# Performance work log

Measured on AMD Instinct MI355X. Metric: run time of the kernel, lower is better.

Reference implementation:

```python
import jax, jax.numpy as jnp
import numpy as np

K = 128            # knowledge_n == stu_dim == prednet_input_len
EXER = 16384       # exer_n
N = K + EXER       # entity count
B = 4096           # batch of students
E = 400000         # edges per graph
T = B * 50         # packed history length (avg 50 interactions/student)


def setup_inputs() -> dict:
    key = jax.random.key(0)
    ks = jax.random.split(key, 24)
    f = lambda i, shape: jax.random.normal(ks[i], shape, dtype=jnp.float32) * 0.05
    inp = {
        # learned parameters
        'entity_emb': f(0, (N, K)),
        'gcn_W': f(1, (3, 4, K, K)),          # 3 graphs x 4 layers
        'gcn_b': jnp.zeros((3, 4, K), jnp.float32),
        'full_stu_W': f(2, (2 * K,)),          # Linear(2K -> 1) weight
        'full_stu_b': f(3, ()),
        'full_exer_W': f(4, (2 * K,)),
        'full_exer_b': f(5, ()),
        'disc_emb': f(6, (EXER, 1)),           # e_discrimination embedding
        'W1': f(7, (K, 512)), 'b1': jnp.zeros((512,), jnp.float32),
        'W2': f(8, (512, 216)), 'b2': jnp.zeros((216,), jnp.float32),
        'W3': f(9, (216, 1)), 'b3': jnp.zeros((1,), jnp.float32),
        # graph structure (local_map), edge lists over all N entities
        'sim_src': jax.random.randint(ks[10], (E,), 0, N),
        'sim_dst': jax.random.randint(ks[11], (E,), 0, N),
        'pre_src': jax.random.randint(ks[12], (E,), 0, N),
        'pre_dst': jax.random.randint(ks[13], (E,), 0, N),
        'ec_src': jax.random.randint(ks[14], (E,), 0, N),
        'ec_dst': jax.random.randint(ks[15], (E,), 0, N),
        # forward args
        'stu_id': jax.random.randint(ks[16], (B,), 0, 8192),
        'exer_id': jax.random.randint(ks[17], (B,), 0, EXER),
        'kn_emb': jax.random.uniform(ks[18], (B, K), dtype=jnp.float32),
        'history_ids': jax.random.randint(ks[19], (T,), 0, EXER),
        'history_segids': jnp.sort(jax.random.randint(ks[20], (T,), 0, B)),
    }
    return inp


def _edge_norm(src, dst, n):
    ones = jnp.ones(src.shape[0], jnp.float32)
    deg_o = jax.ops.segment_sum(ones, src, num_segments=n)
    deg_i = jax.ops.segment_sum(ones, dst, num_segments=n)
    return jax.lax.rsqrt(jnp.maximum(deg_o[src], 1.0) * jnp.maximum(deg_i[dst], 1.0))


def reference(entity_emb, gcn_W, gcn_b, full_stu_W, full_stu_b, full_exer_W,
              full_exer_b, disc_emb, W1, b1, W2, b2, W3, b3,
              sim_src, sim_dst, pre_src, pre_dst, ec_src, ec_dst,
              stu_id, exer_id, kn_emb, history_ids, history_segids):
    graphs = [(sim_src, sim_dst), (pre_src, pre_dst), (ec_src, ec_dst)]
    norms = [_edge_norm(s, d, N) for s, d in graphs]

    # 4-layer, 3-graph GCN diffusion over entity embeddings
    embs = [entity_emb]
    h = entity_emb
    for l in range(4):
        nh = jnp.zeros_like(h)
        for g, (s, d) in enumerate(graphs):
            agg = jax.ops.segment_sum(h[s] * norms[g][:, None], d, num_segments=N)
            nh = nh + agg @ gcn_W[g, l] + gcn_b[g, l]
        h = nh
        embs.append(h)
    stack = jnp.stack(embs)                       # [5, N, K]
    full = jnp.mean(stack, axis=0)
    disc_full = jnp.mean(stack[3:], axis=0)       # discarding_layers=2 -> layers 3,4

    concept = full[:K]                            # [K, K]
    exer_ent = full[K:]                           # [EXER, K]
    stu_exe = disc_full[K:]                       # [EXER, K]

    # ragged per-student history gather + mean (packed segment reduce)
    Bn = stu_id.shape[0]
    ssum = jax.ops.segment_sum(stu_exe[history_ids], history_segids, num_segments=Bn)
    cnt = jax.ops.segment_sum(jnp.ones(history_ids.shape[0], jnp.float32),
                              history_segids, num_segments=Bn)
    stu = ssum / jnp.maximum(cnt, 1.0)[:, None]   # [B, K]

    exer = exer_ent[exer_id]                      # [B, K]

    # broadcast bilinear: cat(repeat(x), kn_vector) @ W  ==  xWa + conceptWb + b
    prof = jax.nn.sigmoid((stu @ full_stu_W[:K])[:, None]
                          + (concept @ full_stu_W[K:])[None, :] + full_stu_b)
    diff = jax.nn.sigmoid((exer @ full_exer_W[:K])[:, None]
                          + (concept @ full_exer_W[K:])[None, :] + full_exer_b)
    e_disc = jax.nn.sigmoid(disc_emb[exer_id]) * 10.0   # [B, 1]

    x = e_disc * (prof - diff) * kn_emb           # [B, K]
    x = jax.nn.sigmoid(x @ W1 + b1)
    x = jax.nn.sigmoid(x @ W2 + b2)
    return jax.nn.sigmoid(x @ W3 + b3)            # [B, 1]
```

## Files before the change

### kernel.cpp

```cpp
#include <hip/hip_runtime.h>

constexpr int KDIM  = 128;
constexpr int NEXER = 16384;
constexpr int NNODE = KDIM + NEXER;
constexpr int NEDGE = 400000;
constexpr int NBATCH = 4096;
constexpr int NHIST = NBATCH * 50;

constexpr int NCHUNK = 32;
constexpr int CHSZ   = NEDGE / NCHUNK;
constexpr int RHALF  = NNODE / 2;

typedef __attribute__((ext_vector_type(8))) short bf16x8;
typedef __attribute__((ext_vector_type(4))) float f32x4;

__device__ __forceinline__ float sigmoidf(float x) {
    return 1.0f / (1.0f + __expf(-x));
}

__device__ __forceinline__ ushort f2bf(float f) {
    uint x = __float_as_uint(f);
    uint r = (x + 0x7FFFu + ((x >> 16) & 1u)) >> 16;
    return (ushort)r;
}

__device__ __forceinline__ void accum8(float* ax, uint4 p, float w) {
    ax[0] += w * __uint_as_float(p.x << 16);
    ax[1] += w * __uint_as_float(p.x & 0xFFFF0000u);
    ax[2] += w * __uint_as_float(p.y << 16);
    ax[3] += w * __uint_as_float(p.y & 0xFFFF0000u);
    ax[4] += w * __uint_as_float(p.z << 16);
    ax[5] += w * __uint_as_float(p.z & 0xFFFF0000u);
    ax[6] += w * __uint_as_float(p.w << 16);
    ax[7] += w * __uint_as_float(p.w & 0xFFFF0000u);
}

__global__ __launch_bounds__(256) void prep_emb_kernel(
    const float* __restrict__ entity, ushort* __restrict__ h_bf,
    float* __restrict__ full_acc)
{
    int idx = blockIdx.x * 256 + threadIdx.x;
    if (idx >= NNODE * KDIM / 2) return;
    float2 v = ((const float2*)entity)[idx];
    ((float2*)full_acc)[idx] = v;
    ((uint*)h_bf)[idx] = (uint)f2bf(v.x) | ((uint)f2bf(v.y) << 16);
}

__global__ __launch_bounds__(256) void prep_w_kernel(
    const float* __restrict__ W, ushort* __restrict__ Wt)
{
    __shared__ float tile[32][33];
    int gl = blockIdx.y;
    int tk = blockIdx.x >> 2, tn = blockIdx.x & 3;
    int k0 = tk * 32, n0 = tn * 32;
    int tx = threadIdx.x & 31, ty = threadIdx.x >> 5;
    const float* src = W + ((size_t)gl << 14);
    #pragma unroll
    for (int i = 0; i < 4; ++i) {
        int k = ty * 4 + i;
        tile[k][tx] = src[(k0 + k) * 128 + n0 + tx];
    }
    __syncthreads();
    ushort* dst = Wt + ((size_t)gl << 14);
    #pragma unroll
    for (int i = 0; i < 4; ++i) {
        int n = ty * 4 + i;
        dst[(n0 + n) * 128 + k0 + tx] = f2bf(tile[tx][n]);
    }
}

__global__ __launch_bounds__(256) void prep_head_kernel(
    const float* __restrict__ W1, const float* __restrict__ W2,
    ushort* __restrict__ W1t, ushort* __restrict__ W2t)
{
    int idx = blockIdx.x * 256 + threadIdx.x;
    if (idx < 512 * 128) {
        int n = idx >> 7, k = idx & 127;
        W1t[idx] = f2bf(W1[k * 512 + n]);
    }
    int idx2 = idx - 512 * 128;
    if (idx2 >= 0 && idx2 < 224 * 512) {
        int n = idx2 >> 9, k = idx2 & 511;
        W2t[idx2] = f2bf(n < 216 ? W2[k * 216 + n] : 0.f);
    }
}

__global__ __launch_bounds__(256) void count_part_kernel(
    const int* __restrict__ s0, const int* __restrict__ d0,
    const int* __restrict__ s1, const int* __restrict__ d1,
    const int* __restrict__ s2, const int* __restrict__ d2,
    int* __restrict__ partial,
    ushort* __restrict__ rank)
{
    __shared__ int hist[RHALF];
    int c = blockIdx.x, r = blockIdx.y, gs = blockIdx.z;
    const int* arr = (gs == 0) ? s0 : (gs == 1) ? d0 : (gs == 2) ? s1
                   : (gs == 3) ? d1 : (gs == 4) ? s2 : d2;
    for (int i = threadIdx.x; i < RHALF; i += 256) hist[i] = 0;
    __syncthreads();
    int base = r * RHALF;
    const int* p = arr + c * CHSZ;
    if (gs & 1) {
        ushort* rk = rank + (size_t)(gs >> 1) * NEDGE + c * CHSZ;
        for (int i = threadIdx.x; i < CHSZ; i += 256) {
            int v = p[i] - base;
            if ((unsigned)v < (unsigned)RHALF)
                rk[i] = (ushort)atomicAdd(&hist[v], 1);
        }
    } else {
        for (int i = threadIdx.x; i < CHSZ; i += 256) {
            int v = p[i] - base;
            if ((unsigned)v < (unsigned)RHALF) atomicAdd(&hist[v], 1);
        }
    }
    __syncthreads();
    int* outp = partial + ((size_t)gs * NCHUNK + c) * NNODE + base;
    for (int i = threadIdx.x; i < RHALF; i += 256) outp[i] = hist[i];
}

__global__ __launch_bounds__(256) void sum_kernel(
    const int* __restrict__ partial, int* __restrict__ cnt)
{
    int idx = blockIdx.x * 256 + threadIdx.x;
    if (idx >= 6 * NNODE) return;
    int gs = idx / NNODE, node = idx - gs * NNODE;
    const int* pp = partial + (size_t)gs * NCHUNK * NNODE + node;
    int s = 0;
    #pragma unroll
    for (int c = 0; c < NCHUNK; ++c) s += pp[c * NNODE];
    cnt[idx] = s;
}

__global__ __launch_bounds__(256) void scan_kernel(
    const int* __restrict__ cnt, int* __restrict__ rp)
{
    int g = blockIdx.x;
    const int* c = cnt + (g * 2 + 1) * NNODE;
    int* r = rp + g * (NNODE + 1);
    __shared__ int part[256];
    int t = threadIdx.x;
    constexpr int CH = (NNODE + 255) / 256;
    int lo = t * CH;
    int hi = lo + CH; if (hi > NNODE) hi = NNODE;
    int s = 0;
    for (int i = lo; i < hi; ++i) s += c[i];
    part[t] = s;
    __syncthreads();
    for (int off = 1; off < 256; off <<= 1) {
        int v = part[t];
        if (t >= off) v += part[t - off];
        __syncthreads();
        part[t] = v;
        __syncthreads();
    }
    int run = (t == 0) ? 0 : part[t - 1];
    for (int i = lo; i < hi; ++i) { r[i] = run; run += c[i]; }
    if (t == 255) r[NNODE] = part[255];
}

__global__ __launch_bounds__(256) void base_kernel(
    const int* __restrict__ partial, const int* __restrict__ rp,
    int* __restrict__ chunk_base)
{
    int idx = blockIdx.x * 256 + threadIdx.x;
    if (idx >= 3 * NNODE) return;
    int g = idx / NNODE, node = idx - g * NNODE;
    int running = rp[g * (NNODE + 1) + node];
    const int* pp = partial + (size_t)(g * 2 + 1) * NCHUNK * NNODE + node;
    int* ob = chunk_base + (size_t)g * NCHUNK * NNODE + node;
    #pragma unroll
    for (int c = 0; c < NCHUNK; ++c) { ob[c * NNODE] = running; running += pp[c * NNODE]; }
}

__global__ __launch_bounds__(256) void fill_scatter_kernel(
    const int* __restrict__ s0, const int* __restrict__ d0,
    const int* __restrict__ s1, const int* __restrict__ d1,
    const int* __restrict__ s2, const int* __restrict__ d2,
    const int* __restrict__ cnt, const int* __restrict__ chunk_base,
    const ushort* __restrict__ rank, int2* __restrict__ csr_packed)
{
    int e = blockIdx.x * 256 + threadIdx.x;
    int g = blockIdx.y;
    if (e >= NEDGE) return;
    const int* s = (g == 0) ? s0 : (g == 1) ? s1 : s2;
    const int* d = (g == 0) ? d0 : (g == 1) ? d1 : d2;
    int sv = s[e], dv = d[e];
    int c = e / CHSZ;
    int pos = chunk_base[((size_t)g * NCHUNK + c) * NNODE + dv]
            + (int)rank[(size_t)g * NEDGE + e];
    int a = cnt[(g * 2 + 0) * NNODE + sv]; if (a < 1) a = 1;
    int b = cnt[(g * 2 + 1) * NNODE + dv]; if (b < 1) b = 1;
    float w = rsqrtf((float)a * (float)b);
    csr_packed[(size_t)g * NEDGE + pos] = make_int2(sv, __float_as_int(w));
}

__global__ __launch_bounds__(256) void gather_kernel(
    const ushort* __restrict__ h_bf, const int2* __restrict__ csr_packed,
    const int* __restrict__ rp, ushort* __restrict__ agg)
{
    int t = threadIdx.x;
    int wave = t >> 6, lane = t & 63;
    int sub = lane >> 4, li = lane & 15;
    int g = blockIdx.y;
    int row = blockIdx.x * 16 + wave * 4 + sub;
    int js = rp[g * (NNODE + 1) + row];
    int je = rp[g * (NNODE + 1) + row + 1];
    const int2* ep = csr_packed + (size_t)g * NEDGE;
    const uint4* hb4 = (const uint4*)h_bf;
    float ax[8];
    #pragma unroll
    for (int i = 0; i < 8; ++i) ax[i] = 0.f;
    int j = js;
    if (j + 3 < je) {
        int2 eA0 = ep[j], eA1 = ep[j + 1], eA2 = ep[j + 2], eA3 = ep[j + 3];
        uint4 pA0 = hb4[(size_t)eA0.x * 16 + li];
        uint4 pA1 = hb4[(size_t)eA1.x * 16 + li];
        uint4 pA2 = hb4[(size_t)eA2.x * 16 + li];
        uint4 pA3 = hb4[(size_t)eA3.x * 16 + li];
        j += 4;
        while (j + 3 < je) {
            int2 eB0 = ep[j], eB1 = ep[j + 1], eB2 = ep[j + 2], eB3 = ep[j + 3];
            uint4 pB0 = hb4[(size_t)eB0.x * 16 + li];
            uint4 pB1 = hb4[(size_t)eB1.x * 16 + li];
            uint4 pB2 = hb4[(size_t)eB2.x * 16 + li];
            uint4 pB3 = hb4[(size_t)eB3.x * 16 + li];
            accum8(ax, pA0, __int_as_float(eA0.y));
            accum8(ax, pA1, __int_as_float(eA1.y));
            accum8(ax, pA2, __int_as_float(eA2.y));
            accum8(ax, pA3, __int_as_float(eA3.y));
            eA0 = eB0; eA1 = eB1; eA2 = eB2; eA3 = eB3;
            pA0 = pB0; pA1 = pB1; pA2 = pB2; pA3 = pB3;
            j += 4;
        }
        accum8(ax, pA0, __int_as_float(eA0.y));
        accum8(ax, pA1, __int_as_float(eA1.y));
        accum8(ax, pA2, __int_as_float(eA2.y));
        accum8(ax, pA3, __int_as_float(eA3.y));
    }
    for (; j < je; ++j) {
        int2 e0 = ep[j];
        uint4 p0 = hb4[(size_t)e0.x * 16 + li];
        accum8(ax, p0, __int_as_float(e0.y));
    }
    uint4 o;
    o.x = (uint)f2bf(ax[0]) | ((uint)f2bf(ax[1]) << 16);
    o.y = (uint)f2bf(ax[2]) | ((uint)f2bf(ax[3]) << 16);
    o.z = (uint)f2bf(ax[4]) | ((uint)f2bf(ax[5]) << 16);
    o.w = (uint)f2bf(ax[6]) | ((uint)f2bf(ax[7]) << 16);
    ((uint4*)agg)[((size_t)g * NNODE + row) * 16 + li] = o;
}

__global__ __launch_bounds__(256) void gemm_kernel(
    const ushort* __restrict__ agg, const ushort* __restrict__ Wt,
    const float* __restrict__ gcnB, int layer,
    ushort* __restrict__ h_bf, float* __restrict__ full_acc,
    float* __restrict__ disc_acc)
{
    __shared__ ushort Wlds[128 * 136];
    __shared__ float bsum[128];
    int t = threadIdx.x;
    int wave = t >> 6, lane = t & 63;
    int R0 = blockIdx.x * 64;
    if (t < 128)
        bsum[t] = gcnB[(0 * 4 + layer) * 128 + t] + gcnB[(1 * 4 + layer) * 128 + t]
                + gcnB[(2 * 4 + layer) * 128 + t];
    int m = lane & 15, q = lane >> 4;
    int arow = R0 + wave * 16 + m;
    f32x4 acc[8];
    #pragma unroll
    for (int n = 0; n < 8; ++n) acc[n] = (f32x4){0.f, 0.f, 0.f, 0.f};
    for (int g = 0; g < 3; ++g) {
        __syncthreads();
        const ushort* src = Wt + ((size_t)(g * 4 + layer) << 14);
        for (int i = t; i < 2048; i += 256) {
            int row = i >> 4, c = i & 15;
            *(uint4*)&Wlds[row * 136 + c * 8] = *(const uint4*)(src + row * 128 + c * 8);
        }
        __syncthreads();
        const ushort* ap = agg + ((size_t)g * NNODE + arow) * 128 + q * 8;
        bf16x8 af[4];
        #pragma unroll
        for (int k = 0; k < 4; ++k) af[k] = *(const bf16x8*)(ap + k * 32);
        #pragma unroll
        for (int n = 0; n < 8; ++n) {
            const ushort* bp = &Wlds[(n * 16 + m) * 136 + q * 8];
            #pragma unroll
            for (int k = 0; k < 4; ++k) {
                bf16x8 bfr = *(const bf16x8*)(bp + k * 32);
                acc[n] = __builtin_amdgcn_mfma_f32_16x16x32_bf16(af[k], bfr, acc[n], 0, 0, 0);
            }
        }
    }
    __syncthreads();
    float* stage = (float*)Wlds;
    #pragma unroll
    for (int n = 0; n < 8; ++n) {
        #pragma unroll
        for (int r = 0; r < 4; ++r)
            stage[(wave * 16 + q * 4 + r) * 128 + n * 16 + m] = acc[n][r];
    }
    __syncthreads();
    for (int idx = t; idx < 64 * 128; idx += 256) {
        int row = idx >> 7, col = idx & 127;
        int gr = R0 + row;
        float v = stage[idx] + bsum[col];
        size_t o = (size_t)gr * 128 + col;
        full_acc[o] += v;
        h_bf[o] = f2bf(v);
        if (gr >= KDIM) {
            size_t od = (size_t)(gr - KDIM) * 128 + col;
            if (layer == 2) disc_acc[od] = v;
            else if (layer == 3) disc_acc[od] += v;
        }
    }
}

__global__ __launch_bounds__(256) void scale_kernel(
    float* __restrict__ full_acc, const float* __restrict__ disc_acc,
    ushort* __restrict__ disc_bf)
{
    constexpr int NK4 = NNODE * KDIM / 4;
    constexpr int DK4 = NEXER * KDIM / 4;
    int idx = blockIdx.x * blockDim.x + threadIdx.x;
    if (idx < NK4) {
        float4 v = ((float4*)full_acc)[idx];
        v.x *= 0.2f; v.y *= 0.2f; v.z *= 0.2f; v.w *= 0.2f;
        ((float4*)full_acc)[idx] = v;
    } else if (idx < NK4 + DK4) {
        int i = idx - NK4;
        float4 v = ((const float4*)disc_acc)[i];
        uint2 o;
        o.x = (uint)f2bf(v.x * 0.5f) | ((uint)f2bf(v.y * 0.5f) << 16);
        o.y = (uint)f2bf(v.z * 0.5f) | ((uint)f2bf(v.w * 0.5f) << 16);
        ((uint2*)disc_bf)[i] = o;
    }
}

__global__ __launch_bounds__(256) void starts_kernel(
    const int* __restrict__ segids, int* __restrict__ starts)
{
    int i = blockIdx.x * blockDim.x + threadIdx.x;
    if (i > NBATCH) return;
    int lo = 0, hi = NHIST;
    while (lo < hi) {
        int m = (lo + hi) >> 1;
        if (segids[m] < i) lo = m + 1; else hi = m;
    }
    starts[i] = lo;
}

__global__ __launch_bounds__(256) void stu_kernel(
    const ushort* __restrict__ disc_bf, const int* __restrict__ hist,
    const int* __restrict__ starts, float* __restrict__ stu)
{
    int t = threadIdx.x;
    int wave = t >> 6, lane = t & 63;
    int sub = lane >> 4, li = lane & 15;
    int b = blockIdx.x * 16 + wave * 4 + sub;
    int js = starts[b], je = starts[b + 1];
    const uint4* db4 = (const uint4*)disc_bf;
    float ax[8];
    #pragma unroll
    for (int i = 0; i < 8; ++i) ax[i] = 0.f;
    int j = js;
    if (j + 3 < je) {
        int i0 = hist[j], i1 = hist[j + 1], i2 = hist[j + 2], i3 = hist[j + 3];
        uint4 pA0 = db4[(size_t)i0 * 16 + li];
        uint4 pA1 = db4[(size_t)i1 * 16 + li];
        uint4 pA2 = db4[(size_t)i2 * 16 + li];
        uint4 pA3 = db4[(size_t)i3 * 16 + li];
        j += 4;
        while (j + 3 < je) {
            int n0 = hist[j], n1 = hist[j + 1], n2 = hist[j + 2], n3 = hist[j + 3];
            uint4 pB0 = db4[(size_t)n0 * 16 + li];
            uint4 pB1 = db4[(size_t)n1 * 16 + li];
            uint4 pB2 = db4[(size_t)n2 * 16 + li];
            uint4 pB3 = db4[(size_t)n3 * 16 + li];
            accum8(ax, pA0, 1.f); accum8(ax, pA1, 1.f);
            accum8(ax, pA2, 1.f); accum8(ax, pA3, 1.f);
            pA0 = pB0; pA1 = pB1; pA2 = pB2; pA3 = pB3;
            j += 4;
        }
        accum8(ax, pA0, 1.f); accum8(ax, pA1, 1.f);
        accum8(ax, pA2, 1.f); accum8(ax, pA3, 1.f);
    }
    for (; j < je; ++j) {
        uint4 p = db4[(size_t)hist[j] * 16 + li];
        accum8(ax, p, 1.f);
    }
    float c = (float)(je - js); if (c < 1.f) c = 1.f;
    float inv = 1.f / c;
    float4 o0 = {ax[0] * inv, ax[1] * inv, ax[2] * inv, ax[3] * inv};
    float4 o1 = {ax[4] * inv, ax[5] * inv, ax[6] * inv, ax[7] * inv};
    *(float4*)&stu[(size_t)b * KDIM + li * 8] = o0;
    *(float4*)&stu[(size_t)b * KDIM + li * 8 + 4] = o1;
}

__global__ __launch_bounds__(256) void cw_kernel(
    const float* __restrict__ full, const float* __restrict__ fsW,
    const float* __restrict__ feW, float* __restrict__ cw)
{
    int t = threadIdx.x;
    int j = t & 127;
    const float* w = (t < 128) ? (fsW + KDIM) : (feW + KDIM);
    const float* row = full + (size_t)j * KDIM;
    float s = 0.f;
    for (int k = 0; k < KDIM; ++k) s += row[k] * w[k];
    cw[t] = s;
}

__global__ __launch_bounds__(256) void final_kernel(
    const float* __restrict__ stu, const float* __restrict__ full,
    const float* __restrict__ cw,
    const float* __restrict__ fsW, const float* __restrict__ fsB,
    const float* __restrict__ feW, const float* __restrict__ feB,
    const float* __restrict__ disc_emb, const int* __restrict__ exer_id,
    const float* __restrict__ kn,
    const ushort* __restrict__ W1t, const float* __restrict__ b1,
    const ushort* __restrict__ W2t, const float* __restrict__ b2,
    const float* __restrict__ W3, const float* __restrict__ b3,
    float* __restrict__ out)
{
    __shared__ ushort xsl[16][136];
    __shared__ ushort o1l[16][520];
    __shared__ float  o2l[16][228];
    int t = threadIdx.x, wave = t >> 6, lane = t & 63;
    int b0 = blockIdx.x * 16;
    float fsb = fsB[0], feb = feB[0];
    #pragma unroll
    for (int i = 0; i < 4; ++i) {
        int rr = wave * 4 + i;
        int b = b0 + rr;
        int eid = exer_id[b];
        const float* sr = stu + (size_t)b * KDIM;
        const float* er = full + (size_t)(KDIM + eid) * KDIM;
        float sd = sr[lane] * fsW[lane] + sr[lane + 64] * fsW[lane + 64];
        float ed = er[lane] * feW[lane] + er[lane + 64] * feW[lane + 64];
        #pragma unroll
        for (int o = 32; o > 0; o >>= 1) {
            sd += __shfl_xor(sd, o);
            ed += __shfl_xor(ed, o);
        }
        float edisc = 10.f * sigmoidf(disc_emb[eid]);
        for (int j = lane; j < KDIM; j += 64) {
            float prof = sigmoidf(sd + cw[j] + fsb);
            float diff = sigmoidf(ed + cw[KDIM + j] + feb);
            xsl[rr][j] = f2bf(edisc * (prof - diff) * kn[(size_t)b * KDIM + j]);
        }
    }
    __syncthreads();
    int m = lane & 15, q = lane >> 4;
    bf16x8 af[4];
    #pragma unroll
    for (int kk = 0; kk < 4; ++kk) af[kk] = *(const bf16x8*)&xsl[m][kk * 32 + q * 8];
    f32x4 acc[8];
    #pragma unroll
    for (int n = 0; n < 8; ++n) acc[n] = (f32x4){0.f, 0.f, 0.f, 0.f};
    const ushort* w1base = W1t + (size_t)(wave * 128) * 128;
    #pragma unroll
    for (int nt = 0; nt < 8; ++nt) {
        const ushort* bp = w1base + (nt * 16 + m) * 128 + q * 8;
        #pragma unroll
        for (int kk = 0; kk < 4; ++kk) {
            bf16x8 bf = *(const bf16x8*)(bp + kk * 32);
            acc[nt] = __builtin_amdgcn_mfma_f32_16x16x32_bf16(af[kk], bf, acc[nt], 0, 0, 0);
        }
    }
    #pragma unroll
    for (int nt = 0; nt < 8; ++nt) {
        int n = wave * 128 + nt * 16 + m;
        float bv = b1[n];
        #pragma unroll
        for (int r = 0; r < 4; ++r)
            o1l[q * 4 + r][n] = f2bf(sigmoidf(acc[nt][r] + bv));
    }
    __syncthreads();
    int ntt = (wave < 2) ? 4 : 3;
    f32x4 acc2[4];
    #pragma unroll
    for (int i = 0; i < 4; ++i) acc2[i] = (f32x4){0.f, 0.f, 0.f, 0.f};
    #pragma unroll 4
    for (int kk = 0; kk < 16; ++kk) {
        bf16x8 a2 = *(const bf16x8*)&o1l[m][kk * 32 + q * 8];
        #pragma unroll
        for (int tt = 0; tt < 4; ++tt) {
            if (tt < ntt) {
                int nt = wave + 4 * tt;
                bf16x8 bf = *(const bf16x8*)(W2t + (size_t)(nt * 16 + m) * 512 + kk * 32 + q * 8);
                acc2[tt] = __builtin_amdgcn_mfma_f32_16x16x32_bf16(a2, bf, acc2[tt], 0, 0, 0);
            }
        }
    }
    #pragma unroll
    for (int tt = 0; tt < 4; ++tt) {
        if (tt < ntt) {
            int nt = wave + 4 * tt;
            int n = nt * 16 + m;
            if (n < 216) {
                float bv = b2[n];
                #pragma unroll
                for (int r = 0; r < 4; ++r)
                    o2l[q * 4 + r][n] = sigmoidf(acc2[tt][r] + bv);
            }
        }
    }
    __syncthreads();
    int sub = lane >> 4, li = lane & 15;
    int rr = wave * 4 + sub;
    float dot = 0.f;
    for (int p = li; p < 216; p += 16) dot += o2l[rr][p] * W3[p];
    #pragma unroll
    for (int o = 8; o > 0; o >>= 1) dot += __shfl_xor(dot, o, 16);
    if (li == 0) out[b0 + rr] = sigmoidf(dot + b3[0]);
}

extern "C" void kernel_launch(void* const* d_in, const int* in_sizes, int n_in,
                              void* d_out, int out_size, void* d_ws, size_t ws_size,
                              hipStream_t stream)
{
    (void)in_sizes; (void)n_in; (void)out_size; (void)ws_size;
    const float* entity = (const float*)d_in[0];
    const float* gcnW   = (const float*)d_in[1];
    const float* gcnB   = (const float*)d_in[2];
    const float* fsW    = (const float*)d_in[3];
    const float* fsB    = (const float*)d_in[4];
    const float* feW    = (const float*)d_in[5];
    const float* feB    = (const float*)d_in[6];
    const float* disc_emb = (const float*)d_in[7];
    const float* W1 = (const float*)d_in[8];
    const float* b1 = (const float*)d_in[9];
    const float* W2 = (const float*)d_in[10];
    const float* b2 = (const float*)d_in[11];
    const float* W3 = (const float*)d_in[12];
    const float* b3 = (const float*)d_in[13];
    const int* s0 = (const int*)d_in[14];
    const int* d0 = (const int*)d_in[15];
    const int* s1 = (const int*)d_in[16];
    const int* d1 = (const int*)d_in[17];
    const int* s2 = (const int*)d_in[18];
    const int* d2 = (const int*)d_in[19];
    const int* exer_id = (const int*)d_in[21];
    const float* kn = (const float*)d_in[22];
    const int* hist = (const int*)d_in[23];
    const int* segid = (const int*)d_in[24];
    float* out = (float*)d_out;

    char* wsb = (char*)d_ws;
    size_t off = 0;
    auto alloc = [&](size_t bytes) -> void* {
        void* p = wsb + off;
        off = (off + bytes + 255) & ~(size_t)255;
        return p;
    };
    int*    partial   = (int*)alloc((size_t)6 * NCHUNK * NNODE * sizeof(int));
    int*    cnt       = (int*)alloc((size_t)6 * NNODE * sizeof(int));
    int*    rp        = (int*)alloc((size_t)3 * (NNODE + 1) * sizeof(int));
    int*    chunk_base= (int*)alloc((size_t)3 * NCHUNK * NNODE * sizeof(int));
    ushort* rank      = (ushort*)alloc((size_t)3 * NEDGE * sizeof(ushort));
    int2*   csr_packed= (int2*)alloc((size_t)3 * NEDGE * sizeof(int2));
    ushort* h_bf      = (ushort*)alloc((size_t)NNODE * KDIM * sizeof(ushort));
    ushort* agg       = (ushort*)alloc((size_t)3 * NNODE * KDIM * sizeof(ushort));
    ushort* Wt        = (ushort*)alloc((size_t)3 * 4 * KDIM * KDIM * sizeof(ushort));
    ushort* W1t       = (ushort*)alloc((size_t)512 * 128 * sizeof(ushort));
    ushort* W2t       = (ushort*)alloc((size_t)224 * 512 * sizeof(ushort));
    float*  full_acc  = (float*)alloc((size_t)NNODE * KDIM * sizeof(float));
    float*  disc_acc  = (float*)alloc((size_t)NEXER * KDIM * sizeof(float));
    ushort* disc_bf   = (ushort*)alloc((size_t)NEXER * KDIM * sizeof(ushort));
    float*  stu       = (float*)alloc((size_t)NBATCH * KDIM * sizeof(float));
    int*    starts    = (int*)alloc((size_t)(NBATCH + 1) * sizeof(int));
    float*  cw        = (float*)alloc(256 * sizeof(float));

    prep_emb_kernel<<<(NNODE * KDIM / 2 + 255) / 256, 256, 0, stream>>>(entity, h_bf, full_acc);
    prep_w_kernel<<<dim3(16, 12), 256, 0, stream>>>(gcnW, Wt);
    prep_head_kernel<<<(512 * 128 + 224 * 512 + 255) / 256, 256, 0, stream>>>(W1, W2, W1t, W2t);

    count_part_kernel<<<dim3(NCHUNK, 2, 6), 256, 0, stream>>>(s0, d0, s1, d1, s2, d2,
                                                              partial, rank);
    sum_kernel<<<(6 * NNODE + 255) / 256, 256, 0, stream>>>(partial, cnt);
    scan_kernel<<<3, 256, 0, stream>>>(cnt, rp);
    base_kernel<<<(3 * NNODE + 255) / 256, 256, 0, stream>>>(partial, rp, chunk_base);
    fill_scatter_kernel<<<dim3((NEDGE + 255) / 256, 3), 256, 0, stream>>>(
        s0, d0, s1, d1, s2, d2, cnt, chunk_base, rank, csr_packed);

    for (int l = 0; l < 4; ++l) {
        gather_kernel<<<dim3(NNODE / 16, 3), 256, 0, stream>>>(h_bf, csr_packed, rp, agg);
        gemm_kernel<<<NNODE / 64, 256, 0, stream>>>(agg, Wt, gcnB, l, h_bf, full_acc, disc_acc);
    }

    constexpr int SCALE_ELEMS = NNODE * KDIM / 4 + NEXER * KDIM / 4;
    scale_kernel<<<(SCALE_ELEMS + 255) / 256, 256, 0, stream>>>(full_acc, disc_acc, disc_bf);
    starts_kernel<<<(NBATCH + 1 + 255) / 256, 256, 0, stream>>>(segid, starts);
    stu_kernel<<<NBATCH / 16, 256, 0, stream>>>(disc_bf, hist, starts, stu);
    cw_kernel<<<1, 256, 0, stream>>>(full_acc, fsW, feW, cw);
    final_kernel<<<NBATCH / 16, 256, 0, stream>>>(stu, full_acc, cw, fsW, fsB, feW, feB,
                                                  disc_emb, exer_id, kn,
                                                  W1t, b1, W2t, b2, W3, b3, out);
}
```

Measured before the change: 474.6 us.

## Deepen gather prefetch, merge prep kernels, fuse starts search, double edge chunks

Merges the three prep kernels into one launch and folds the history-start binary search into scale_kernel, removing two launches. Doubles NCHUNK so the edge count/scatter pass runs across more blocks, at the cost of a larger partial-histogram buffer and longer per-node sums. Deepens the gather and student-history loops so edge indices are loaded two groups ahead of the row loads. Edge-list loads and aggregate stores use nontemporal hints to reduce cache pollution.

```diff
diff --git a/kernel.cpp b/kernel.cpp
--- a/kernel.cpp
+++ b/kernel.cpp
@@ -7,12 +7,28 @@
 constexpr int NBATCH = 4096;
 constexpr int NHIST = NBATCH * 50;
 
-constexpr int NCHUNK = 32;
+constexpr int NCHUNK = 64;
 constexpr int CHSZ   = NEDGE / NCHUNK;
 constexpr int RHALF  = NNODE / 2;
 
 typedef __attribute__((ext_vector_type(8))) short bf16x8;
 typedef __attribute__((ext_vector_type(4))) float f32x4;
+typedef __attribute__((ext_vector_type(4))) uint u32x4;
+
+#if __has_builtin(__builtin_nontemporal_load)
+#define NT_LOAD_LL(p) __builtin_nontemporal_load(p)
+#else
+#define NT_LOAD_LL(p) (*(p))
+#endif
+
+__device__ __forceinline__ void nt_store_u4(uint4 v, void* p) {
+    u32x4 x = {v.x, v.y, v.z, v.w};
+#if __has_builtin(__builtin_nontemporal_store)
+    __builtin_nontemporal_store(x, (u32x4*)p);
+#else
+    *(u32x4*)p = x;
+#endif
+}
 
 __device__ __forceinline__ float sigmoidf(float x) {
     return 1.0f / (1.0f + __expf(-x));
@@ -24,7 +40,8 @@
     return (ushort)r;
 }
 
-__device__ __forceinline__ void accum8(float* ax, uint4 p, float w) {
+__device__ __forceinline__ void accum8(float* ax, uint4 p, int wbits) {
+    float w = __int_as_float(wbits);
     ax[0] += w * __uint_as_float(p.x << 16);
     ax[1] += w * __uint_as_float(p.x & 0xFFFF0000u);
     ax[2] += w * __uint_as_float(p.y << 16);
@@ -35,45 +52,50 @@
     ax[7] += w * __uint_as_float(p.w & 0xFFFF0000u);
 }
 
-__global__ __launch_bounds__(256) void prep_emb_kernel(
+constexpr int EMB_BLOCKS = (NNODE * KDIM / 2) / 256;
+constexpr int W_BLOCKS   = 16 * 12;
+constexpr int HEAD_ELEMS = 512 * 128 + 224 * 512;
+constexpr int HEAD_BLOCKS = (HEAD_ELEMS + 255) / 256;
+__global__ __launch_bounds__(256) void prep_all_kernel(
     const float* __restrict__ entity, ushort* __restrict__ h_bf,
-    float* __restrict__ full_acc)
-{
-    int idx = blockIdx.x * 256 + threadIdx.x;
-    if (idx >= NNODE * KDIM / 2) return;
-    float2 v = ((const float2*)entity)[idx];
-    ((float2*)full_acc)[idx] = v;
-    ((uint*)h_bf)[idx] = (uint)f2bf(v.x) | ((uint)f2bf(v.y) << 16);
-}
-
-__global__ __launch_bounds__(256) void prep_w_kernel(
-    const float* __restrict__ W, ushort* __restrict__ Wt)
-{
-    __shared__ float tile[32][33];
-    int gl = blockIdx.y;
-    int tk = blockIdx.x >> 2, tn = blockIdx.x & 3;
-    int k0 = tk * 32, n0 = tn * 32;
-    int tx = threadIdx.x & 31, ty = threadIdx.x >> 5;
-    const float* src = W + ((size_t)gl << 14);
-    #pragma unroll
-    for (int i = 0; i < 4; ++i) {
-        int k = ty * 4 + i;
-        tile[k][tx] = src[(k0 + k) * 128 + n0 + tx];
-    }
-    __syncthreads();
-    ushort* dst = Wt + ((size_t)gl << 14);
-    #pragma unroll
-    for (int i = 0; i < 4; ++i) {
-        int n = ty * 4 + i;
-        dst[(n0 + n) * 128 + k0 + tx] = f2bf(tile[tx][n]);
-    }
-}
-
-__global__ __launch_bounds__(256) void prep_head_kernel(
+    float* __restrict__ full_acc,
+    const float* __restrict__ W, ushort* __restrict__ Wt,
     const float* __restrict__ W1, const float* __restrict__ W2,
     ushort* __restrict__ W1t, ushort* __restrict__ W2t)
 {
-    int idx = blockIdx.x * 256 + threadIdx.x;
+    __shared__ float tile[32][33];
+    int bx = blockIdx.x;
+    if (bx < EMB_BLOCKS) {
+        int idx = bx * 256 + threadIdx.x;
+        float2 v = ((const float2*)entity)[idx];
+        ((float2*)full_acc)[idx] = v;
+        ((uint*)h_bf)[idx] = (uint)f2bf(v.x) | ((uint)f2bf(v.y) << 16);
+        return;
+    }
+    bx -= EMB_BLOCKS;
+    if (bx < W_BLOCKS) {
+        int gl = bx >> 4;
+        int tl = bx & 15;
+        int tk = tl >> 2, tn = tl & 3;
+        int k0 = tk * 32, n0 = tn * 32;
+        int tx = threadIdx.x & 31, ty = threadIdx.x >> 5;
+        const float* src = W + ((size_t)gl << 14);
+        #pragma unroll
+        for (int i = 0; i < 4; ++i) {
+            int k = ty * 4 + i;
+            tile[k][tx] = src[(k0 + k) * 128 + n0 + tx];
+        }
+        __syncthreads();
+        ushort* dst = Wt + ((size_t)gl << 14);
+        #pragma unroll
+        for (int i = 0; i < 4; ++i) {
+            int n = ty * 4 + i;
+            dst[(n0 + n) * 128 + k0 + tx] = f2bf(tile[tx][n]);
+        }
+        return;
+    }
+    bx -= W_BLOCKS;
+    int idx = bx * 256 + threadIdx.x;
     if (idx < 512 * 128) {
         int n = idx >> 7, k = idx & 127;
         W1t[idx] = f2bf(W1[k * 512 + n]);
@@ -126,7 +148,7 @@
     int gs = idx / NNODE, node = idx - gs * NNODE;
     const int* pp = partial + (size_t)gs * NCHUNK * NNODE + node;
     int s = 0;
-    #pragma unroll
+    #pragma unroll 8
     for (int c = 0; c < NCHUNK; ++c) s += pp[c * NNODE];
     cnt[idx] = s;
 }
@@ -168,7 +190,7 @@
     int running = rp[g * (NNODE + 1) + node];
     const int* pp = partial + (size_t)(g * 2 + 1) * NCHUNK * NNODE + node;
     int* ob = chunk_base + (size_t)g * NCHUNK * NNODE + node;
-    #pragma unroll
+    #pragma unroll 8
     for (int c = 0; c < NCHUNK; ++c) { ob[c * NNODE] = running; running += pp[c * NNODE]; }
 }
 
@@ -210,44 +232,52 @@
     float ax[8];
     #pragma unroll
     for (int i = 0; i < 8; ++i) ax[i] = 0.f;
+    auto ld2 = [&](int idx) -> int2 {
+        long long v = NT_LOAD_LL((const long long*)(ep + idx));
+        int2 r; r.x = (int)(unsigned)v; r.y = (int)(v >> 32); return r;
+    };
     int j = js;
-    if (j + 3 < je) {
-        int2 eA0 = ep[j], eA1 = ep[j + 1], eA2 = ep[j + 2], eA3 = ep[j + 3];
-        uint4 pA0 = hb4[(size_t)eA0.x * 16 + li];
-        uint4 pA1 = hb4[(size_t)eA1.x * 16 + li];
-        uint4 pA2 = hb4[(size_t)eA2.x * 16 + li];
-        uint4 pA3 = hb4[(size_t)eA3.x * 16 + li];
-        j += 4;
+    if (je - js >= 8) {
+        int2 a0 = ld2(j), a1 = ld2(j + 1), a2 = ld2(j + 2), a3 = ld2(j + 3);
+        int2 b0 = ld2(j + 4), b1 = ld2(j + 5), b2 = ld2(j + 6), b3 = ld2(j + 7);
+        uint4 ra0 = hb4[(size_t)a0.x * 16 + li];
+        uint4 ra1 = hb4[(size_t)a1.x * 16 + li];
+        uint4 ra2 = hb4[(size_t)a2.x * 16 + li];
+        uint4 ra3 = hb4[(size_t)a3.x * 16 + li];
+        j += 8;
         while (j + 3 < je) {
-            int2 eB0 = ep[j], eB1 = ep[j + 1], eB2 = ep[j + 2], eB3 = ep[j + 3];
-            uint4 pB0 = hb4[(size_t)eB0.x * 16 + li];
-            uint4 pB1 = hb4[(size_t)eB1.x * 16 + li];
-            uint4 pB2 = hb4[(size_t)eB2.x * 16 + li];
-            uint4 pB3 = hb4[(size_t)eB3.x * 16 + li];
-            accum8(ax, pA0, __int_as_float(eA0.y));
-            accum8(ax, pA1, __int_as_float(eA1.y));
-            accum8(ax, pA2, __int_as_float(eA2.y));
-            accum8(ax, pA3, __int_as_float(eA3.y));
-            eA0 = eB0; eA1 = eB1; eA2 = eB2; eA3 = eB3;
-            pA0 = pB0; pA1 = pB1; pA2 = pB2; pA3 = pB3;
+            int2 c0 = ld2(j), c1 = ld2(j + 1), c2 = ld2(j + 2), c3 = ld2(j + 3);
+            uint4 rb0 = hb4[(size_t)b0.x * 16 + li];
+            uint4 rb1 = hb4[(size_t)b1.x * 16 + li];
+            uint4 rb2 = hb4[(size_t)b2.x * 16 + li];
+            uint4 rb3 = hb4[(size_t)b3.x * 16 + li];
+            accum8(ax, ra0, a0.y); accum8(ax, ra1, a1.y);
+            accum8(ax, ra2, a2.y); accum8(ax, ra3, a3.y);
+            a0 = b0; a1 = b1; a2 = b2; a3 = b3;
+            b0 = c0; b1 = c1; b2 = c2; b3 = c3;
+            ra0 = rb0; ra1 = rb1; ra2 = rb2; ra3 = rb3;
             j += 4;
         }
-        accum8(ax, pA0, __int_as_float(eA0.y));
-        accum8(ax, pA1, __int_as_float(eA1.y));
-        accum8(ax, pA2, __int_as_float(eA2.y));
-        accum8(ax, pA3, __int_as_float(eA3.y));
+        uint4 rb0 = hb4[(size_t)b0.x * 16 + li];
+        uint4 rb1 = hb4[(size_t)b1.x * 16 + li];
+        uint4 rb2 = hb4[(size_t)b2.x * 16 + li];
+        uint4 rb3 = hb4[(size_t)b3.x * 16 + li];
+        accum8(ax, ra0, a0.y); accum8(ax, ra1, a1.y);
+        accum8(ax, ra2, a2.y); accum8(ax, ra3, a3.y);
+        accum8(ax, rb0, b0.y); accum8(ax, rb1, b1.y);
+        accum8(ax, rb2, b2.y); accum8(ax, rb3, b3.y);
     }
     for (; j < je; ++j) {
         int2 e0 = ep[j];
         uint4 p0 = hb4[(size_t)e0.x * 16 + li];
-        accum8(ax, p0, __int_as_float(e0.y));
+        accum8(ax, p0, e0.y);
     }
     uint4 o;
     o.x = (uint)f2bf(ax[0]) | ((uint)f2bf(ax[1]) << 16);
     o.y = (uint)f2bf(ax[2]) | ((uint)f2bf(ax[3]) << 16);
     o.z = (uint)f2bf(ax[4]) | ((uint)f2bf(ax[5]) << 16);
     o.w = (uint)f2bf(ax[6]) | ((uint)f2bf(ax[7]) << 16);
-    ((uint4*)agg)[((size_t)g * NNODE + row) * 16 + li] = o;
+    nt_store_u4(o, (uint4*)agg + ((size_t)g * NNODE + row) * 16 + li);
 }
 
 __global__ __launch_bounds__(256) void gemm_kernel(
@@ -317,7 +347,8 @@
 
 __global__ __launch_bounds__(256) void scale_kernel(
     float* __restrict__ full_acc, const float* __restrict__ disc_acc,
-    ushort* __restrict__ disc_bf)
+    ushort* __restrict__ disc_bf, const int* __restrict__ segids,
+    int* __restrict__ starts)
 {
     constexpr int NK4 = NNODE * KDIM / 4;
     constexpr int DK4 = NEXER * KDIM / 4;
@@ -334,19 +365,14 @@
         o.y = (uint)f2bf(v.z * 0.5f) | ((uint)f2bf(v.w * 0.5f) << 16);
         ((uint2*)disc_bf)[i] = o;
     }
-}
-
-__global__ __launch_bounds__(256) void starts_kernel(
-    const int* __restrict__ segids, int* __restrict__ starts)
-{
-    int i = blockIdx.x * blockDim.x + threadIdx.x;
-    if (i > NBATCH) return;
-    int lo = 0, hi = NHIST;
-    while (lo < hi) {
-        int m = (lo + hi) >> 1;
-        if (segids[m] < i) lo = m + 1; else hi = m;
-    }
-    starts[i] = lo;
+    if (idx <= NBATCH) {
+        int lo = 0, hi = NHIST;
+        while (lo < hi) {
+            int m = (lo + hi) >> 1;
+            if (segids[m] < idx) lo = m + 1; else hi = m;
+        }
+        starts[idx] = lo;
+    }
 }
 
 __global__ __launch_bounds__(256) void stu_kernel(
@@ -362,31 +388,40 @@
     float ax[8];
     #pragma unroll
     for (int i = 0; i < 8; ++i) ax[i] = 0.f;
+    int one = __float_as_int(1.0f);
     int j = js;
-    if (j + 3 < je) {
-        int i0 = hist[j], i1 = hist[j + 1], i2 = hist[j + 2], i3 = hist[j + 3];
-        uint4 pA0 = db4[(size_t)i0 * 16 + li];
-        uint4 pA1 = db4[(size_t)i1 * 16 + li];
-        uint4 pA2 = db4[(size_t)i2 * 16 + li];
-        uint4 pA3 = db4[(size_t)i3 * 16 + li];
-        j += 4;
+    if (je - js >= 8) {
+        int a0 = hist[j], a1 = hist[j + 1], a2 = hist[j + 2], a3 = hist[j + 3];
+        int b0 = hist[j + 4], b1 = hist[j + 5], b2 = hist[j + 6], b3 = hist[j + 7];
+        uint4 ra0 = db4[(size_t)a0 * 16 + li];
+        uint4 ra1 = db4[(size_t)a1 * 16 + li];
+        uint4 ra2 = db4[(size_t)a2 * 16 + li];
+        uint4 ra3 = db4[(size_t)a3 * 16 + li];
+        j += 8;
         while (j + 3 < je) {
-            int n0 = hist[j], n1 = hist[j + 1], n2 = hist[j + 2], n3 = hist[j + 3];
-            uint4 pB0 = db4[(size_t)n0 * 16 + li];
-            uint4 pB1 = db4[(size_t)n1 * 16 + li];
-            uint4 pB2 = db4[(size_t)n2 * 16 + li];
-            uint4 pB3 = db4[(size_t)n3 * 16 + li];
-            accum8(ax, pA0, 1.f); accum8(ax, pA1, 1.f);
-            accum8(ax, pA2, 1.f); accum8(ax, pA3, 1.f);
-            pA0 = pB0; pA1 = pB1; pA2 = pB2; pA3 = pB3;
+            int c0 = hist[j], c1 = hist[j + 1], c2 = hist[j + 2], c3 = hist[j + 3];
+            uint4 rb0 = db4[(size_t)b0 * 16 + li];
+            uint4 rb1 = db4[(size_t)b1 * 16 + li];
+            uint4 rb2 = db4[(size_t)b2 * 16 + li];
+            uint4 rb3 = db4[(size_t)b3 * 16 + li];
+            accum8(ax, ra0, one); accum8(ax, ra1, one);
+            accum8(ax, ra2, one); accum8(ax, ra3, one);
+            b0 = c0; b1 = c1; b2 = c2; b3 = c3;
+            ra0 = rb0; ra1 = rb1; ra2 = rb2; ra3 = rb3;
             j += 4;
         }
-        accum8(ax, pA0, 1.f); accum8(ax, pA1, 1.f);
-        accum8(ax, pA2, 1.f); accum8(ax, pA3, 1.f);
+        uint4 rb0 = db4[(size_t)b0 * 16 + li];
+        uint4 rb1 = db4[(size_t)b1 * 16 + li];
+        uint4 rb2 = db4[(size_t)b2 * 16 + li];
+        uint4 rb3 = db4[(size_t)b3 * 16 + li];
+        accum8(ax, ra0, one); accum8(ax, ra1, one);
+        accum8(ax, ra2, one); accum8(ax, ra3, one);
+        accum8(ax, rb0, one); accum8(ax, rb1, one);
+        accum8(ax, rb2, one); accum8(ax, rb3, one);
     }
     for (; j < je; ++j) {
         uint4 p = db4[(size_t)hist[j] * 16 + li];
-        accum8(ax, p, 1.f);
+        accum8(ax, p, one);
     }
     float c = (float)(je - js); if (c < 1.f) c = 1.f;
     float inv = 1.f / c;
@@ -570,9 +605,8 @@
     int*    starts    = (int*)alloc((size_t)(NBATCH + 1) * sizeof(int));
     float*  cw        = (float*)alloc(256 * sizeof(float));
 
-    prep_emb_kernel<<<(NNODE * KDIM / 2 + 255) / 256, 256, 0, stream>>>(entity, h_bf, full_acc);
-    prep_w_kernel<<<dim3(16, 12), 256, 0, stream>>>(gcnW, Wt);
-    prep_head_kernel<<<(512 * 128 + 224 * 512 + 255) / 256, 256, 0, stream>>>(W1, W2, W1t, W2t);
+    prep_all_kernel<<<EMB_BLOCKS + W_BLOCKS + HEAD_BLOCKS, 256, 0, stream>>>(
+        entity, h_bf, full_acc, gcnW, Wt, W1, W2, W1t, W2t);
 
     count_part_kernel<<<dim3(NCHUNK, 2, 6), 256, 0, stream>>>(s0, d0, s1, d1, s2, d2,
                                                               partial, rank);
@@ -588,8 +622,8 @@
     }
 
     constexpr int SCALE_ELEMS = NNODE * KDIM / 4 + NEXER * KDIM / 4;
-    scale_kernel<<<(SCALE_ELEMS + 255) / 256, 256, 0, stream>>>(full_acc, disc_acc, disc_bf);
-    starts_kernel<<<(NBATCH + 1 + 255) / 256, 256, 0, stream>>>(segid, starts);
+    scale_kernel<<<(SCALE_ELEMS + 255) / 256, 256, 0, stream>>>(full_acc, disc_acc, disc_bf,
+                                                                segid, starts);
     stu_kernel<<<NBATCH / 16, 256, 0, stream>>>(disc_bf, hist, starts, stu);
     cw_kernel<<<1, 256, 0, stream>>>(full_acc, fsW, feW, cw);
     final_kernel<<<NBATCH / 16, 256, 0, stream>>>(stu, full_acc, cw, fsW, fsB, feW, feB,
```

Measured after the change: 499.9 us. 5.3% more time.
